# Kernel optimization log

Measured on AMD Instinct MI355X. Metric: run time of the kernel, lower is better.

The kernel has to match this reference:

```python
import jax, jax.numpy as jnp
import numpy as np

T = 15          # fixed window length from docstring
CENTER = 7      # center_idx
MAXL = 8        # max_len_f = max_len_b = 8
B, D, H = 8192, 512, 512


def _gru_final(x, lengths, Wih, Whh, bih, bhh):
    """Run a GRU over x (B, L, D) and return the hidden state after each
    sample's own `lengths` steps (packed-sequence final-hidden semantics)."""
    Bn, L, _ = x.shape
    Hn = Whh.shape[1]
    # Precompute input projections for all timesteps: (B, L, 3H)
    xp = jnp.einsum('bld,gd->blg', x, Wih) + bih
    mask = jnp.arange(L)[None, :] < lengths[:, None]  # (B, L) valid steps

    def step(h, inp):
        xp_t, m_t = inp                      # (B,3H), (B,)
        gh = h @ Whh.T + bhh                 # (B,3H)
        xr, xz, xn = jnp.split(xp_t, 3, axis=-1)
        hr, hz, hn = jnp.split(gh, 3, axis=-1)
        r = jax.nn.sigmoid(xr + hr)
        z = jax.nn.sigmoid(xz + hz)
        n = jnp.tanh(xn + r * hn)
        h_new = (1.0 - z) * n + z * h
        h = jnp.where(m_t[:, None], h_new, h)  # freeze h past sequence end
        return h, None

    h0 = jnp.zeros((Bn, Hn), x.dtype)
    hT, _ = jax.lax.scan(step, h0, (jnp.moveaxis(xp, 0, 1)[:L], mask.T))
    return hT


def setup_inputs() -> dict:
    key = jax.random.key(0)
    ks = jax.random.split(key, 16)
    s_ih = 1.0 / np.sqrt(H)
    u = lambda k, shape: jax.random.uniform(k, shape, jnp.float32, -s_ih, s_ih)
    inp = {
        'padded_window': jax.random.normal(ks[0], (B, T, D), jnp.float32),
        'window_len': jax.random.randint(ks[1], (B,), 1, T + 1, jnp.int32),
        # forward GRU params (PyTorch layout: gates ordered r,z,n)
        'Wih_f': u(ks[2], (3 * H, D)), 'Whh_f': u(ks[3], (3 * H, H)),
        'bih_f': u(ks[4], (3 * H,)),   'bhh_f': u(ks[5], (3 * H,)),
        # backward GRU params
        'Wih_b': u(ks[6], (3 * H, D)), 'Whh_b': u(ks[7], (3 * H, H)),
        'bih_b': u(ks[8], (3 * H,)),   'bhh_b': u(ks[9], (3 * H,)),
        # MLP: Linear(2H,H) -> ReLU -> Linear(H,H)
        'W1': u(ks[10], (H, 2 * H)), 'b1': u(ks[11], (H,)),
        'W2': u(ks[12], (H, H)),     'b2': u(ks[13], (H,)),
    }
    return inp


def reference(padded_window, window_len, Wih_f, Whh_f, bih_f, bhh_f,
              Wih_b, Whh_b, bih_b, bhh_b, W1, b1, W2, b2):
    len_f = (window_len - 1) // 2 + 1   # (B,)
    len_b = window_len // 2 + 1         # (B,)
    j = jnp.arange(MAXL)
    # forward sub-sequence: window[center-l_f+1 : center+1]
    idx_f = jnp.clip(CENTER - len_f[:, None] + 1 + j[None, :], 0, T - 1)
    # backward sub-sequence: flip(window[center : center+l_b]) -> descending idx
    idx_b = jnp.clip(CENTER + len_b[:, None] - 1 - j[None, :], 0, T - 1)
    xf = jnp.take_along_axis(padded_window, idx_f[:, :, None], axis=1)  # (B,8,D)
    xb = jnp.take_along_axis(padded_window, idx_b[:, :, None], axis=1)  # (B,8,D)
    h_f = _gru_final(xf, len_f, Wih_f, Whh_f, bih_f, bhh_f)
    h_b = _gru_final(xb, len_b, Wih_b, Whh_b, bih_b, bhh_b)
    combined = jnp.concatenate([h_f, h_b], axis=1)  # (B, 2H)
    hidden = jax.nn.relu(combined @ W1.T + b1)
    return hidden @ W2.T + b2
```

## Files before the change

kernel.cpp:

```cpp
#include <hip/hip_runtime.h>

typedef unsigned short u16;
typedef __attribute__((ext_vector_type(4))) float f32x4;
typedef __attribute__((ext_vector_type(8))) __bf16 bf16x8;
typedef __attribute__((ext_vector_type(8))) u16 u16x8;
typedef __attribute__((ext_vector_type(4))) u16 u16x4;
typedef __attribute__((ext_vector_type(4))) int i32x4;

#define MFMA(a, b, c) __builtin_amdgcn_mfma_f32_16x16x32_bf16(a, b, c, 0, 0, 0)

__device__ __forceinline__ u16 f2bf(float f) {
  union { float f; unsigned u; } v; v.f = f;
  unsigned r = v.u + 0x7FFFu + ((v.u >> 16) & 1u);
  return (u16)(r >> 16);
}
__device__ __forceinline__ float bf2f(u16 b) {
  union { unsigned u; float f; } v; v.u = ((unsigned)b) << 16; return v.f;
}
__device__ __forceinline__ float sigm(float x) { return 1.f / (1.f + __expf(-x)); }
__device__ __forceinline__ float tanh_(float x) {
  float e = __expf(-2.f * fabsf(x));
  float r = (1.f - e) / (1.f + e);
  return x < 0.f ? -r : r;
}

#define GSTRIDE 131072

__global__ __launch_bounds__(256) void cvt_bf16(const float* __restrict__ src,
                                                u16* __restrict__ dst, int n8) {
  int i = blockIdx.x * 256 + threadIdx.x;
  if (i >= n8) return;
  int e = i * 8;
  u16x8 o;
#pragma unroll
  for (int j = 0; j < 8; ++j) o[j] = f2bf(src[e + j]);
  *(u16x8*)(dst + e) = o;
}

__global__ __launch_bounds__(256) void wrepack(const float* __restrict__ Whh,
                                               u16* __restrict__ Wp) {
  int i = blockIdx.x * 256 + threadIdx.x;
  if (i >= 98304) return;
  int q = i / 3072;
  int r1 = i % 3072;
  int kk = r1 / 192;
  int r2 = r1 % 192;
  int g = r2 / 64;
  int r3 = r2 % 64;
  int ks = r3 >> 4, ln = r3 & 15;
  const float* src =
      Whh + (size_t)(g * 512 + q * 16 + ln) * 512 + kk * 32 + ks * 8;
  u16x8 o;
#pragma unroll
  for (int j = 0; j < 8; ++j) o[j] = f2bf(src[j]);
  *(u16x8*)(Wp + (size_t)i * 8) = o;
}

#define LROWA 520

__global__ __launch_bounds__(256)
__attribute__((amdgpu_waves_per_eu(1, 1))) void xp_gemm(
    const float* __restrict__ win, const int* __restrict__ wlen,
    const u16* __restrict__ Wihb_f, const u16* __restrict__ Wihb_b,
    const float* __restrict__ bih_f, const float* __restrict__ bih_b,
    const float* __restrict__ bhh_f, const float* __restrict__ bhh_b,
    u16* __restrict__ xp) {
  extern __shared__ char smem[];
  u16* As = (u16*)smem;

  const int dir = blockIdx.y;
  const u16* Wb = dir ? Wihb_b : Wihb_f;
  const float* bih = dir ? bih_b : bih_f;
  const float* bhh = dir ? bhh_b : bhh_f;

  const int tid = threadIdx.x;
  const int bx = blockIdx.x;

  {
    const int r = tid >> 1, hh = tid & 1;
    const int m = bx * 128 + r;
    const int s = m >> 3, tt = m & 7;
    const int wl = wlen[s];
    const int len = dir ? (wl / 2 + 1) : ((wl - 1) / 2 + 1);
    const int widx = dir ? (6 + len - tt) : (8 - len + tt);
    const float* src = win + ((size_t)s * 15 + widx) * 512 + hh * 256;
    u16* dst = As + r * LROWA + hh * 256;
#pragma unroll
    for (int i = 0; i < 32; ++i) {
      f32x4 v0 = *(const f32x4*)(src + i * 8);
      f32x4 v1 = *(const f32x4*)(src + i * 8 + 4);
      u16x8 o;
      o[0] = f2bf(v0[0]); o[1] = f2bf(v0[1]); o[2] = f2bf(v0[2]); o[3] = f2bf(v0[3]);
      o[4] = f2bf(v1[0]); o[5] = f2bf(v1[1]); o[6] = f2bf(v1[2]); o[7] = f2bf(v1[3]);
      *(u16x8*)(dst + i * 8) = o;
    }
  }
  __syncthreads();

  const int wave = tid >> 6;
  const int lane = tid & 63;
  const int ln = lane & 15;
  const int ks = lane >> 4;

#pragma unroll 1
  for (int g = 0; g < 6; ++g) {
    const int c0 = wave * 24 + g * 4;

    f32x4 acc[8][4];
#pragma unroll
    for (int mt = 0; mt < 8; ++mt)
#pragma unroll
      for (int u = 0; u < 4; ++u)
#pragma unroll
        for (int j = 0; j < 4; ++j) acc[mt][u][j] = 0.f;

#pragma unroll
    for (int kk = 0; kk < 16; ++kk) {
      const int krel = kk * 32 + ks * 8;
      bf16x8 a[8];
#pragma unroll
      for (int mt = 0; mt < 8; ++mt)
        a[mt] = *(const bf16x8*)(As + (mt * 16 + ln) * LROWA + krel);
      bf16x8 b[4];
#pragma unroll
      for (int u = 0; u < 4; ++u)
        b[u] = *(const bf16x8*)(Wb + (size_t)((c0 + u) * 16 + ln) * 512 + krel);
#pragma unroll
      for (int mt = 0; mt < 8; ++mt)
#pragma unroll
        for (int u = 0; u < 4; ++u) acc[mt][u] = MFMA(a[mt], b[u], acc[mt][u]);
    }

#pragma unroll
    for (int u = 0; u < 4; ++u) {
      const int col = (c0 + u) * 16 + ln;
      const float bv = bih[col] + (col < 1024 ? bhh[col] : 0.f);
#pragma unroll
      for (int mt = 0; mt < 8; ++mt)
#pragma unroll
        for (int j = 0; j < 4; ++j) {
          const int rowm = bx * 128 + mt * 16 + ks * 4 + j;
          const int s = rowm >> 3, t = rowm & 7;
          const size_t idx = ((size_t)(dir * 8 + t) * 96 + (c0 + u)) * GSTRIDE +
                             (size_t)(s >> 2) * 64 + ln * 4 + (s & 3);
          xp[idx] = f2bf(acc[mt][u][j] + bv);
        }
    }
  }
}

#define LROW 520

__global__ __launch_bounds__(1024)
__attribute__((amdgpu_waves_per_eu(4, 4))) void gru_rec(
    const int* __restrict__ wlen, const u16* __restrict__ Wp_f,
    const u16* __restrict__ Wp_b, const float* __restrict__ bhh_f,
    const float* __restrict__ bhh_b, const u16* __restrict__ xp,
    u16* __restrict__ hcat) {
  extern __shared__ char smem[];
  u16* hb0 = (u16*)smem;
  u16* hb1 = hb0 + 64 * LROW;
  int* len_s = (int*)(hb1 + 64 * LROW);
  int* bmax_s = len_s + 64;

  const int dir = blockIdx.x & 1;
  const int grp = blockIdx.x >> 1;
  const int s0 = grp * 64;
  const u16* W = dir ? Wp_b : Wp_f;
  const float* bhh = dir ? bhh_b : bhh_f;

  const int tid = threadIdx.x;
  const int wave = tid >> 6;
  const int lane = tid & 63;
  const int ln = lane & 15;
  const int ks = lane >> 4;

  if (tid == 0) *bmax_s = 0;
  for (int i = tid; i < 64 * LROW / 8; i += 1024) ((u16x8*)hb0)[i] = (u16x8)0;
  __syncthreads();
  if (tid < 64) {
    int wl = wlen[s0 + tid];
    int len = dir ? (wl / 2 + 1) : ((wl - 1) / 2 + 1);
    len_s[tid] = len;
    atomicMax(bmax_s, len);
  }
  __syncthreads();
  const int bmax = *bmax_s;

  float b_hn[2];
#pragma unroll
  for (int p = 0; p < 2; ++p) b_hn[p] = bhh[1024 + (p * 16 + wave) * 16 + ln];

  for (int t = 0; t < bmax; ++t) {
    u16* h_cur = (t & 1) ? hb1 : hb0;
    u16* h_nxt = (t & 1) ? hb0 : hb1;
    const u16* xpt = xp + (size_t)(dir * 8 + t) * 96 * GSTRIDE;

#pragma unroll
    for (int p = 0; p < 2; ++p) {
      const int q = p * 16 + wave;
      const int dcol = q * 16 + ln;
      const u16* wq = W + (size_t)q * 24576 + lane * 8;

      u16x4 xr4[4], xz4[4], xn4[4];
#pragma unroll
      for (int mt = 0; mt < 4; ++mt) {
        const size_t off = (size_t)((s0 >> 2) + mt * 4 + ks) * 64 + ln * 4;
        xr4[mt] = *(const u16x4*)(xpt + (size_t)q * GSTRIDE + off);
        xz4[mt] = *(const u16x4*)(xpt + (size_t)(32 + q) * GSTRIDE + off);
        xn4[mt] = *(const u16x4*)(xpt + (size_t)(64 + q) * GSTRIDE + off);
      }

      f32x4 accr[4], accz[4], acchn[4];
#pragma unroll
      for (int mt = 0; mt < 4; ++mt)
#pragma unroll
        for (int j = 0; j < 4; ++j) {
          accr[mt][j] = 0.f; accz[mt][j] = 0.f; acchn[mt][j] = 0.f;
        }

#pragma unroll
      for (int kk = 0; kk < 16; ++kk) {
        const int krel = kk * 32 + ks * 8;
        bf16x8 a[4];
#pragma unroll
        for (int mt = 0; mt < 4; ++mt)
          a[mt] = *(const bf16x8*)(h_cur + (mt * 16 + ln) * LROW + krel);
        const u16* wk = wq + kk * 1536;
        bf16x8 br = *(const bf16x8*)(wk);
        bf16x8 bz = *(const bf16x8*)(wk + 512);
        bf16x8 bn = *(const bf16x8*)(wk + 1024);
#pragma unroll
        for (int mt = 0; mt < 4; ++mt) {
          accr[mt] = MFMA(a[mt], br, accr[mt]);
          accz[mt] = MFMA(a[mt], bz, accz[mt]);
          acchn[mt] = MFMA(a[mt], bn, acchn[mt]);
        }
      }

#pragma unroll
      for (int mt = 0; mt < 4; ++mt)
#pragma unroll
        for (int j = 0; j < 4; ++j) {
          const int row = mt * 16 + ks * 4 + j;
          float xr = bf2f(xr4[mt][j]);
          float xz = bf2f(xz4[mt][j]);
          float xn = bf2f(xn4[mt][j]);
          float rr = sigm(accr[mt][j] + xr);
          float zz = sigm(accz[mt][j] + xz);
          float nn = tanh_(xn + rr * (acchn[mt][j] + b_hn[p]));
          float hold = bf2f(h_cur[row * LROW + dcol]);
          float hnew = (t < len_s[row]) ? ((1.f - zz) * nn + zz * hold) : hold;
          h_nxt[row * LROW + dcol] = f2bf(hnew);
        }
    }
    __syncthreads();
  }

  const u16* hf = (bmax & 1) ? hb1 : hb0;
  const int xrow = tid >> 4;
  const int xcol = tid & 15;
#pragma unroll
  for (int i = 0; i < 4; ++i) {
    int off = (i * 16 + xcol) * 8;
    u16x8 v = *(const u16x8*)(hf + xrow * LROW + off);
    __builtin_nontemporal_store(
        v, (u16x8*)(hcat + (size_t)(s0 + xrow) * 1024 + dir * 512 + off));
  }
}

__global__ __launch_bounds__(256) void build_wcat(const float* __restrict__ Whh,
                                                  const float* __restrict__ Wih,
                                                  u16* __restrict__ Wcat) {
  int i = blockIdx.x * 256 + threadIdx.x;
  if (i >= 1536 * 1024 / 8) return;
  int e = i * 8;
  int g = e >> 10, k = e & 1023;
  const float* src = (k < 512) ? (Whh + g * 512 + k) : (Wih + g * 512 + (k - 512));
  u16x8 o;
#pragma unroll
  for (int j = 0; j < 8; ++j) o[j] = f2bf(src[j]);
  *(u16x8*)(Wcat + e) = o;
}

__global__ __launch_bounds__(512)
__attribute__((amdgpu_waves_per_eu(2, 2))) void gru_persistent(
    const float* __restrict__ win, const int* __restrict__ wlen,
    const u16* __restrict__ Wcat_f, const u16* __restrict__ Wcat_b,
    const float* __restrict__ bih_f, const float* __restrict__ bhh_f,
    const float* __restrict__ bih_b, const float* __restrict__ bhh_b,
    u16* __restrict__ hcat) {
  extern __shared__ char smem[];
  u16* h_s = (u16*)smem;
  u16* x_s = (u16*)(smem + 64 * LROW * 2);
  int* len_s = (int*)(smem + 2 * 64 * LROW * 2);
  int* bmax_s = len_s + 64;

  const int dir = blockIdx.x & 1;
  const int grp = blockIdx.x >> 1;
  const int s0 = grp * 64;
  const u16* W = dir ? Wcat_b : Wcat_f;
  const float* bih = dir ? bih_b : bih_f;
  const float* bhh = dir ? bhh_b : bhh_f;

  const int tid = threadIdx.x;
  const int wave = tid >> 6;
  const int lane = tid & 63;
  const int ln = lane & 15;
  const int ks = lane >> 4;

  if (tid == 0) *bmax_s = 0;
  for (int i = tid; i < 64 * LROW / 8; i += 512) ((u16x8*)h_s)[i] = (u16x8)0;
  __syncthreads();
  if (tid < 64) {
    int wl = wlen[s0 + tid];
    int len = dir ? (wl / 2 + 1) : ((wl - 1) / 2 + 1);
    len_s[tid] = len;
    atomicMax(bmax_s, len);
  }
  __syncthreads();
  const int bmax = *bmax_s;

  float b_r[4], b_z[4], b_xn[4], b_hn[4];
#pragma unroll
  for (int p = 0; p < 4; ++p) {
    int d = (p * 8 + wave) * 16 + ln;
    b_r[p] = bih[d] + bhh[d];
    b_z[p] = bih[512 + d] + bhh[512 + d];
    b_xn[p] = bih[1024 + d];
    b_hn[p] = bhh[1024 + d];
  }

  const int xrow = tid >> 3;
  const int xcol = tid & 7;
  const int mylen = len_s[xrow];
  const long xbase = (long)(s0 + xrow) * 15 + (dir ? (6 + mylen) : (8 - mylen));

  for (int t = 0; t < bmax; ++t) {
    {
      long rowidx = dir ? (xbase - t) : (xbase + t);
      const float* src = win + rowidx * 512;
      u16* dst = x_s + xrow * LROW;
#pragma unroll
      for (int i = 0; i < 8; ++i) {
        int off = xcol * 8 + i * 64;
        f32x4 v0 = *(const f32x4*)(src + off);
        f32x4 v1 = *(const f32x4*)(src + off + 4);
        u16x8 o;
        o[0] = f2bf(v0[0]); o[1] = f2bf(v0[1]); o[2] = f2bf(v0[2]); o[3] = f2bf(v0[3]);
        o[4] = f2bf(v1[0]); o[5] = f2bf(v1[1]); o[6] = f2bf(v1[2]); o[7] = f2bf(v1[3]);
        *(u16x8*)(dst + off) = o;
      }
    }
    __syncthreads();

    unsigned holdp[3][4][2];

#pragma unroll
    for (int p = 0; p < 4; ++p) {
      const int dcol = (p * 8 + wave) * 16 + ln;
      const u16* wrow = W + (size_t)dcol * 1024;

      f32x4 accr[4], accz[4], acchn[4], accxn[4];
#pragma unroll
      for (int mt = 0; mt < 4; ++mt)
#pragma unroll
        for (int j = 0; j < 4; ++j) {
          accr[mt][j] = 0.f; accz[mt][j] = 0.f;
          acchn[mt][j] = 0.f; accxn[mt][j] = 0.f;
        }

#pragma unroll
      for (int kk = 0; kk < 16; ++kk) {
        const int krel = kk * 32 + ks * 8;
        bf16x8 a[4];
#pragma unroll
        for (int mt = 0; mt < 4; ++mt)
          a[mt] = *(const bf16x8*)(h_s + (mt * 16 + ln) * LROW + krel);
        bf16x8 br = *(const bf16x8*)(wrow + krel);
        bf16x8 bz = *(const bf16x8*)(wrow + 512 * 1024 + krel);
        bf16x8 bn = *(const bf16x8*)(wrow + 1024 * 1024 + krel);
#pragma unroll
        for (int mt = 0; mt < 4; ++mt) {
          accr[mt] = MFMA(a[mt], br, accr[mt]);
          accz[mt] = MFMA(a[mt], bz, accz[mt]);
          acchn[mt] = MFMA(a[mt], bn, acchn[mt]);
        }
      }
#pragma unroll
      for (int kk = 0; kk < 16; ++kk) {
        const int krel = kk * 32 + ks * 8;
        bf16x8 a[4];
#pragma unroll
        for (int mt = 0; mt < 4; ++mt)
          a[mt] = *(const bf16x8*)(x_s + (mt * 16 + ln) * LROW + krel);
        bf16x8 br = *(const bf16x8*)(wrow + 512 + krel);
        bf16x8 bz = *(const bf16x8*)(wrow + 512 * 1024 + 512 + krel);
        bf16x8 bn = *(const bf16x8*)(wrow + 1024 * 1024 + 512 + krel);
#pragma unroll
        for (int mt = 0; mt < 4; ++mt) {
          accr[mt] = MFMA(a[mt], br, accr[mt]);
          accz[mt] = MFMA(a[mt], bz, accz[mt]);
          accxn[mt] = MFMA(a[mt], bn, accxn[mt]);
        }
      }

      if (p < 3) {
#pragma unroll
        for (int mt = 0; mt < 4; ++mt)
#pragma unroll
          for (int jp = 0; jp < 2; ++jp) {
            unsigned pk = 0;
#pragma unroll
            for (int jh = 0; jh < 2; ++jh) {
              const int j = jp * 2 + jh;
              const int row = mt * 16 + ks * 4 + j;
              float rr = sigm(accr[mt][j] + b_r[p]);
              float zz = sigm(accz[mt][j] + b_z[p]);
              float nn = tanh_(accxn[mt][j] + b_xn[p] +
                               rr * (acchn[mt][j] + b_hn[p]));
              float hold = bf2f(h_s[row * LROW + dcol]);
              float hnew = (t < len_s[row]) ? ((1.f - zz) * nn + zz * hold) : hold;
              pk |= ((unsigned)f2bf(hnew)) << (16 * jh);
            }
            holdp[p][mt][jp] = pk;
          }
      } else {
        __syncthreads();
#pragma unroll
        for (int pp = 0; pp < 3; ++pp) {
          const int dd = (pp * 8 + wave) * 16 + ln;
#pragma unroll
          for (int mt = 0; mt < 4; ++mt)
#pragma unroll
            for (int jp = 0; jp < 2; ++jp) {
              unsigned pk = holdp[pp][mt][jp];
              const int row = mt * 16 + ks * 4 + jp * 2;
              h_s[row * LROW + dd] = (u16)pk;
              h_s[(row + 1) * LROW + dd] = (u16)(pk >> 16);
            }
        }
#pragma unroll
        for (int mt = 0; mt < 4; ++mt)
#pragma unroll
          for (int j = 0; j < 4; ++j) {
            const int row = mt * 16 + ks * 4 + j;
            float rr = sigm(accr[mt][j] + b_r[3]);
            float zz = sigm(accz[mt][j] + b_z[3]);
            float nn = tanh_(accxn[mt][j] + b_xn[3] +
                             rr * (acchn[mt][j] + b_hn[3]));
            float hold = bf2f(h_s[row * LROW + dcol]);
            float hnew = (t < len_s[row]) ? ((1.f - zz) * nn + zz * hold) : hold;
            h_s[row * LROW + dcol] = f2bf(hnew);
          }
      }
    }
  }

  __syncthreads();
#pragma unroll
  for (int i = 0; i < 8; ++i) {
    int off = xcol * 8 + i * 64;
    u16x8 v = *(const u16x8*)(h_s + xrow * LROW + off);
    __builtin_nontemporal_store(
        v, (u16x8*)(hcat + (size_t)(s0 + xrow) * 1024 + dir * 512 + off));
  }
}

__global__ __launch_bounds__(256) void mlp_gemm(const u16* __restrict__ A,
                                                const u16* __restrict__ Bw,
                                                const float* __restrict__ bias,
                                                void* __restrict__ out, int M,
                                                int N, int K, int mode) {
  __shared__ u16 As[128 * 64], Bs[128 * 64];
  const int tid = threadIdx.x;
  const int wave = tid >> 6, lane = tid & 63;
  const int ln = lane & 15, ks = lane >> 4;
  const int wm = wave & 1, wn = wave >> 1;
  const int m0 = blockIdx.x * 128, n0 = blockIdx.y * 128;
  f32x4 acc[4][4];
#pragma unroll
  for (int mt = 0; mt < 4; ++mt)
#pragma unroll
    for (int nt = 0; nt < 4; ++nt)
#pragma unroll
      for (int j = 0; j < 4; ++j) acc[mt][nt][j] = 0.f;

  const int r = tid >> 1, hh = tid & 1;
  for (int k0 = 0; k0 < K; k0 += 64) {
    const i32x4* sa = (const i32x4*)(A + (size_t)(m0 + r) * K + k0 + hh * 32);
    const i32x4* sb = (const i32x4*)(Bw + (size_t)(n0 + r) * K + k0 + hh * 32);
    i32x4* da = (i32x4*)(As + r * 64 + hh * 32);
    i32x4* db = (i32x4*)(Bs + r * 64 + hh * 32);
#pragma unroll
    for (int i = 0; i < 4; ++i) da[i] = sa[i];
#pragma unroll
    for (int i = 0; i < 4; ++i) db[i] = sb[i];
    __syncthreads();
#pragma unroll
    for (int kk = 0; kk < 2; ++kk) {
      bf16x8 af[4], bfm[4];
#pragma unroll
      for (int mt = 0; mt < 4; ++mt)
        af[mt] = *(const bf16x8*)(As + (wm * 64 + mt * 16 + ln) * 64 + kk * 32 + ks * 8);
#pragma unroll
      for (int nt = 0; nt < 4; ++nt)
        bfm[nt] = *(const bf16x8*)(Bs + (wn * 64 + nt * 16 + ln) * 64 + kk * 32 + ks * 8);
#pragma unroll
      for (int mt = 0; mt < 4; ++mt)
#pragma unroll
        for (int nt = 0; nt < 4; ++nt) acc[mt][nt] = MFMA(af[mt], bfm[nt], acc[mt][nt]);
    }
    __syncthreads();
  }

#pragma unroll
  for (int nt = 0; nt < 4; ++nt) {
    int col = n0 + wn * 64 + nt * 16 + ln;
    float bv = bias[col];
#pragma unroll
    for (int mt = 0; mt < 4; ++mt)
#pragma unroll
      for (int j = 0; j < 4; ++j) {
        int row = m0 + wm * 64 + mt * 16 + ks * 4 + j;
        float v = acc[mt][nt][j] + bv;
        if (mode) {
          v = fmaxf(v, 0.f);
          ((u16*)out)[(size_t)row * N + col] = f2bf(v);
        } else {
          ((float*)out)[(size_t)row * N + col] = v;
        }
      }
  }
}

extern "C" void kernel_launch(void* const* d_in, const int* in_sizes, int n_in,
                              void* d_out, int out_size, void* d_ws, size_t ws_size,
                              hipStream_t stream) {
  (void)in_sizes; (void)n_in; (void)out_size;
  const float* win = (const float*)d_in[0];
  const int* wlen = (const int*)d_in[1];
  const float* Wih_f = (const float*)d_in[2];
  const float* Whh_f = (const float*)d_in[3];
  const float* bih_f = (const float*)d_in[4];
  const float* bhh_f = (const float*)d_in[5];
  const float* Wih_b = (const float*)d_in[6];
  const float* Whh_b = (const float*)d_in[7];
  const float* bih_b = (const float*)d_in[8];
  const float* bhh_b = (const float*)d_in[9];
  const float* W1 = (const float*)d_in[10];
  const float* b1 = (const float*)d_in[11];
  const float* W2 = (const float*)d_in[12];
  const float* b2 = (const float*)d_in[13];

  const size_t NEED = 4ull * 1572864 + 1048576 + 524288 + 16777216 + 8388608 +
                      402653184ull;

  if (ws_size >= NEED) {
    char* ws = (char*)d_ws;
    u16* Wp_f = (u16*)ws;   ws += 1572864;
    u16* Wp_b = (u16*)ws;   ws += 1572864;
    u16* Wihb_f = (u16*)ws; ws += 1572864;
    u16* Wihb_b = (u16*)ws; ws += 1572864;
    u16* W1b = (u16*)ws;    ws += 1048576;
    u16* W2b = (u16*)ws;    ws += 524288;
    u16* hcat = (u16*)ws;   ws += 16777216;
    u16* hidden = (u16*)ws; ws += 8388608;
    u16* xp = (u16*)ws;     ws += 402653184;

    wrepack<<<384, 256, 0, stream>>>(Whh_f, Wp_f);
    wrepack<<<384, 256, 0, stream>>>(Whh_b, Wp_b);
    cvt_bf16<<<384, 256, 0, stream>>>(Wih_f, Wihb_f, 98304);
    cvt_bf16<<<384, 256, 0, stream>>>(Wih_b, Wihb_b, 98304);
    cvt_bf16<<<256, 256, 0, stream>>>(W1, W1b, 65536);
    cvt_bf16<<<128, 256, 0, stream>>>(W2, W2b, 32768);

    const int SMEM_XP = 128 * LROWA * 2;
    (void)hipFuncSetAttribute((const void*)xp_gemm,
                              hipFuncAttributeMaxDynamicSharedMemorySize, SMEM_XP);
    xp_gemm<<<dim3(512, 2), 256, SMEM_XP, stream>>>(
        win, wlen, Wihb_f, Wihb_b, bih_f, bih_b, bhh_f, bhh_b, xp);

    const int SMEM = 2 * 64 * LROW * 2 + 64 * 4 + 16;
    (void)hipFuncSetAttribute((const void*)gru_rec,
                              hipFuncAttributeMaxDynamicSharedMemorySize, SMEM);
    gru_rec<<<256, 1024, SMEM, stream>>>(wlen, Wp_f, Wp_b, bhh_f, bhh_b, xp,
                                         hcat);

    mlp_gemm<<<dim3(64, 4), 256, 0, stream>>>(hcat, W1b, b1, hidden, 8192, 512,
                                              1024, 1);
    mlp_gemm<<<dim3(64, 4), 256, 0, stream>>>(hidden, W2b, b2, d_out, 8192, 512,
                                              512, 0);
  } else {
    char* ws = (char*)d_ws;
    u16* Wcat_f = (u16*)ws;  ws += 3145728;
    u16* Wcat_b = (u16*)ws;  ws += 3145728;
    u16* W1b = (u16*)ws;     ws += 1048576;
    u16* W2b = (u16*)ws;     ws += 524288;
    u16* hcat = (u16*)ws;    ws += 16777216;
    u16* hidden = (u16*)ws;  ws += 8388608;

    build_wcat<<<768, 256, 0, stream>>>(Whh_f, Wih_f, Wcat_f);
    build_wcat<<<768, 256, 0, stream>>>(Whh_b, Wih_b, Wcat_b);
    cvt_bf16<<<256, 256, 0, stream>>>(W1, W1b, 65536);
    cvt_bf16<<<128, 256, 0, stream>>>(W2, W2b, 32768);

    const int SMEM = 2 * 64 * LROW * 2 + 64 * 4 + 16;
    (void)hipFuncSetAttribute((const void*)gru_persistent,
                              hipFuncAttributeMaxDynamicSharedMemorySize, SMEM);
    gru_persistent<<<256, 512, SMEM, stream>>>(win, wlen, Wcat_f, Wcat_b, bih_f,
                                               bhh_f, bih_b, bhh_b, hcat);

    mlp_gemm<<<dim3(64, 4), 256, 0, stream>>>(hcat, W1b, b1, hidden, 8192, 512,
                                              1024, 1);
    mlp_gemm<<<dim3(64, 4), 256, 0, stream>>>(hidden, W2b, b2, d_out, 8192, 512,
                                              512, 0);
  }
}
```

Baseline: 1.840 ms.

## Sort sample quads by window length so GRU blocks skip padded steps

Adds a small counting-sort kernel that orders groups of four samples by their maximum window length. Each GRU recurrence block then processes 16 quads with similar lengths, so the per-block step count (bmax) reflects that block's longest sequence rather than nearly always hitting the maximum. xp loads and hcat stores are redirected through the permutation. The cost is an extra tiny kernel launch and scattered, less contiguous xp and hcat accesses.

```diff
diff --git a/kernel.cpp b/kernel.cpp
--- a/kernel.cpp
+++ b/kernel.cpp
@@ -56,6 +56,33 @@
   *(u16x8*)(Wp + (size_t)i * 8) = o;
 }
 
+__global__ __launch_bounds__(1024) void sort_quads(const int* __restrict__ wlen,
+                                                   int* __restrict__ qorder) {
+  __shared__ int cnt[16];
+  __shared__ int off[16];
+  const int tid = threadIdx.x;
+  if (tid < 16) cnt[tid] = 0;
+  __syncthreads();
+  for (int q = tid; q < 2048; q += 1024) {
+    int m = max(max(wlen[q * 4], wlen[q * 4 + 1]),
+                max(wlen[q * 4 + 2], wlen[q * 4 + 3]));
+    atomicAdd(&cnt[m - 1], 1);
+  }
+  __syncthreads();
+  if (tid == 0) {
+    int run = 0;
+#pragma unroll
+    for (int b = 0; b < 15; ++b) { off[b] = run; run += cnt[b]; }
+  }
+  __syncthreads();
+  for (int q = tid; q < 2048; q += 1024) {
+    int m = max(max(wlen[q * 4], wlen[q * 4 + 1]),
+                max(wlen[q * 4 + 2], wlen[q * 4 + 3]));
+    int pos = atomicAdd(&off[m - 1], 1);
+    qorder[pos] = q;
+  }
+}
+
 #define LROWA 520
 
 __global__ __launch_bounds__(256)
@@ -153,19 +180,19 @@
 
 __global__ __launch_bounds__(1024)
 __attribute__((amdgpu_waves_per_eu(4, 4))) void gru_rec(
-    const int* __restrict__ wlen, const u16* __restrict__ Wp_f,
-    const u16* __restrict__ Wp_b, const float* __restrict__ bhh_f,
-    const float* __restrict__ bhh_b, const u16* __restrict__ xp,
-    u16* __restrict__ hcat) {
+    const int* __restrict__ wlen, const int* __restrict__ qorder,
+    const u16* __restrict__ Wp_f, const u16* __restrict__ Wp_b,
+    const float* __restrict__ bhh_f, const float* __restrict__ bhh_b,
+    const u16* __restrict__ xp, u16* __restrict__ hcat) {
   extern __shared__ char smem[];
   u16* hb0 = (u16*)smem;
   u16* hb1 = hb0 + 64 * LROW;
   int* len_s = (int*)(hb1 + 64 * LROW);
   int* bmax_s = len_s + 64;
+  int* qord_s = bmax_s + 1;
 
   const int dir = blockIdx.x & 1;
   const int grp = blockIdx.x >> 1;
-  const int s0 = grp * 64;
   const u16* W = dir ? Wp_b : Wp_f;
   const float* bhh = dir ? bhh_b : bhh_f;
 
@@ -176,16 +203,22 @@
   const int ks = lane >> 4;
 
   if (tid == 0) *bmax_s = 0;
+  if (tid < 16) qord_s[tid] = qorder[grp * 16 + tid];
   for (int i = tid; i < 64 * LROW / 8; i += 1024) ((u16x8*)hb0)[i] = (u16x8)0;
   __syncthreads();
   if (tid < 64) {
-    int wl = wlen[s0 + tid];
+    int sample = qord_s[tid >> 2] * 4 + (tid & 3);
+    int wl = wlen[sample];
     int len = dir ? (wl / 2 + 1) : ((wl - 1) / 2 + 1);
     len_s[tid] = len;
     atomicMax(bmax_s, len);
   }
   __syncthreads();
   const int bmax = *bmax_s;
+
+  int qr[4];
+#pragma unroll
+  for (int mt = 0; mt < 4; ++mt) qr[mt] = qord_s[mt * 4 + ks];
 
   float b_hn[2];
 #pragma unroll
@@ -205,7 +238,7 @@
       u16x4 xr4[4], xz4[4], xn4[4];
 #pragma unroll
       for (int mt = 0; mt < 4; ++mt) {
-        const size_t off = (size_t)((s0 >> 2) + mt * 4 + ks) * 64 + ln * 4;
+        const size_t off = (size_t)qr[mt] * 64 + ln * 4;
         xr4[mt] = *(const u16x4*)(xpt + (size_t)q * GSTRIDE + off);
         xz4[mt] = *(const u16x4*)(xpt + (size_t)(32 + q) * GSTRIDE + off);
         xn4[mt] = *(const u16x4*)(xpt + (size_t)(64 + q) * GSTRIDE + off);
@@ -259,13 +292,14 @@
 
   const u16* hf = (bmax & 1) ? hb1 : hb0;
   const int xrow = tid >> 4;
-  const int xcol = tid & 15;
+  const int xseg = tid & 15;
+  const int sample = qord_s[xrow >> 2] * 4 + (xrow & 3);
 #pragma unroll
   for (int i = 0; i < 4; ++i) {
-    int off = (i * 16 + xcol) * 8;
+    int off = (i * 16 + xseg) * 8;
     u16x8 v = *(const u16x8*)(hf + xrow * LROW + off);
     __builtin_nontemporal_store(
-        v, (u16x8*)(hcat + (size_t)(s0 + xrow) * 1024 + dir * 512 + off));
+        v, (u16x8*)(hcat + (size_t)sample * 1024 + dir * 512 + off));
   }
 }
 
@@ -554,7 +588,7 @@
   const float* b2 = (const float*)d_in[13];
 
   const size_t NEED = 4ull * 1572864 + 1048576 + 524288 + 16777216 + 8388608 +
-                      402653184ull;
+                      402653184ull + 16384;
 
   if (ws_size >= NEED) {
     char* ws = (char*)d_ws;
@@ -566,8 +600,10 @@
     u16* W2b = (u16*)ws;    ws += 524288;
     u16* hcat = (u16*)ws;   ws += 16777216;
     u16* hidden = (u16*)ws; ws += 8388608;
+    int* qorder = (int*)ws; ws += 16384;
     u16* xp = (u16*)ws;     ws += 402653184;
 
+    sort_quads<<<1, 1024, 0, stream>>>(wlen, qorder);
     wrepack<<<384, 256, 0, stream>>>(Whh_f, Wp_f);
     wrepack<<<384, 256, 0, stream>>>(Whh_b, Wp_b);
     cvt_bf16<<<384, 256, 0, stream>>>(Wih_f, Wihb_f, 98304);
@@ -581,11 +617,11 @@
     xp_gemm<<<dim3(512, 2), 256, SMEM_XP, stream>>>(
         win, wlen, Wihb_f, Wihb_b, bih_f, bih_b, bhh_f, bhh_b, xp);
 
-    const int SMEM = 2 * 64 * LROW * 2 + 64 * 4 + 16;
+    const int SMEM = 2 * 64 * LROW * 2 + 64 * 4 + 4 + 16 * 4 + 64;
     (void)hipFuncSetAttribute((const void*)gru_rec,
                               hipFuncAttributeMaxDynamicSharedMemorySize, SMEM);
-    gru_rec<<<256, 1024, SMEM, stream>>>(wlen, Wp_f, Wp_b, bhh_f, bhh_b, xp,
-                                         hcat);
+    gru_rec<<<256, 1024, SMEM, stream>>>(wlen, qorder, Wp_f, Wp_b, bhh_f,
+                                         bhh_b, xp, hcat);
 
     mlp_gemm<<<dim3(64, 4), 256, 0, stream>>>(hcat, W1b, b1, hidden, 8192, 512,
                                               1024, 1);
```

Measured after the change: 1.796 ms. -2.4%, faster.
